# Kernel optimization log

Measured on AMD Instinct MI355X. Metric: run time of the kernel, lower is better.

Reference implementation:

```python
import jax, jax.numpy as jnp
import numpy as np

WEIGHT = 2.0  # penalty weight for |argmax - label| == 1 (original forward arg `weight`)
B, S, C = 64, 8192, 512


def setup_inputs() -> dict:
    key = jax.random.key(0)
    k1, k2 = jax.random.split(key)
    logits = jax.random.normal(k1, (B, S, C), dtype=jnp.float32)
    pre = jax.nn.log_softmax(logits, axis=-1)  # module expects log-softmax inputs
    y_true = jax.random.randint(k2, (B, S), 0, C)
    return {"pre": pre, "y_true": y_true}


def reference(pre, y_true):
    # gather log-prob of the true class: [B, S]
    gathered = jnp.take_along_axis(pre, y_true[..., None], axis=-1)[..., 0]
    # predicted class per position: [B, S]
    pred = jnp.argmax(pre, axis=-1)
    # penalize positions where prediction is off-by-one from the label
    mask = jnp.abs(pred - y_true) == 1
    total = jnp.sum(jnp.where(mask, WEIGHT * gathered, gathered))
    return total / pre.shape[0]
```

## Files before the change

kernel.cpp:

```cpp
#include <hip/hip_runtime.h>

#define NROWS (64 * 8192)
#define C 512
#define WEIGHT 2.0f
#define NBLOCKS 2048
#define BLOCK 256

__global__ __launch_bounds__(BLOCK) void nll_rows_kernel(
    const float* __restrict__ pre,
    const int* __restrict__ y_true,
    float* __restrict__ partial) {
    const int lane = threadIdx.x & 63;
    const int wave = threadIdx.x >> 6;
    const int gwave = blockIdx.x * 4 + wave;
    const int nwaves = gridDim.x * 4;

    float acc = 0.0f;

    for (int row = gwave; row < NROWS; row += nwaves) {
        const float4* rowp = reinterpret_cast<const float4*>(pre + (size_t)row * C);
        float4 a = rowp[lane];
        float4 b = rowp[64 + lane];

        int baseA = lane * 4;
        float mval = a.x; int midx = baseA;
        if (a.y > mval) { mval = a.y; midx = baseA + 1; }
        if (a.z > mval) { mval = a.z; midx = baseA + 2; }
        if (a.w > mval) { mval = a.w; midx = baseA + 3; }
        int baseB = 256 + lane * 4;
        if (b.x > mval) { mval = b.x; midx = baseB; }
        if (b.y > mval) { mval = b.y; midx = baseB + 1; }
        if (b.z > mval) { mval = b.z; midx = baseB + 2; }
        if (b.w > mval) { mval = b.w; midx = baseB + 3; }

        #pragma unroll
        for (int off = 1; off < 64; off <<= 1) {
            float oval = __shfl_xor(mval, off);
            int   oidx = __shfl_xor(midx, off);
            if (oval > mval || (oval == mval && oidx < midx)) {
                mval = oval; midx = oidx;
            }
        }

        int t = y_true[row];
        float g = pre[(size_t)row * C + t];
        int d = midx - t;
        float w = (d == 1 || d == -1) ? WEIGHT : 1.0f;
        if (lane == 0) acc += w * g;
    }

    __shared__ float ssum[4];
    if (lane == 0) ssum[wave] = acc;
    __syncthreads();
    if (threadIdx.x == 0) {
        partial[blockIdx.x] = ssum[0] + ssum[1] + ssum[2] + ssum[3];
    }
}

__global__ __launch_bounds__(256) void nll_reduce_kernel(
    const float* __restrict__ partial, float* __restrict__ out, int n) {
    __shared__ float s[256];
    float acc = 0.0f;
    for (int i = threadIdx.x; i < n; i += 256) acc += partial[i];
    s[threadIdx.x] = acc;
    __syncthreads();
    for (int w = 128; w > 0; w >>= 1) {
        if (threadIdx.x < w) s[threadIdx.x] += s[threadIdx.x + w];
        __syncthreads();
    }
    if (threadIdx.x == 0) out[0] = s[0] * (1.0f / 64.0f);
}

extern "C" void kernel_launch(void* const* d_in, const int* in_sizes, int n_in,
                              void* d_out, int out_size, void* d_ws, size_t ws_size,
                              hipStream_t stream) {
    const float* pre = (const float*)d_in[0];
    const int* y_true = (const int*)d_in[1];
    float* out = (float*)d_out;
    float* partial = (float*)d_ws;

    nll_rows_kernel<<<NBLOCKS, BLOCK, 0, stream>>>(pre, y_true, partial);
    nll_reduce_kernel<<<1, 256, 0, stream>>>(partial, out, NBLOCKS);
}
```

Baseline: 189.9 us.

## Process two rows per wave iteration with nontemporal loads and shuffle gather

Each wave now loads two rows per loop iteration using nontemporal vector loads, raising memory-level parallelism. The true-class log-prob is taken from registers via a wave shuffle instead of a separate global load. The loop trip count becomes a compile-time constant. This adds register pressure and assumes the row count divides evenly.

```diff
diff --git a/kernel.cpp b/kernel.cpp
--- a/kernel.cpp
+++ b/kernel.cpp
@@ -5,6 +5,48 @@
 #define WEIGHT 2.0f
 #define NBLOCKS 2048
 #define BLOCK 256
+#define NWAVES (NBLOCKS * 4)
+#define ITERS (NROWS / (2 * NWAVES))
+
+typedef float v4f __attribute__((ext_vector_type(4)));
+
+__device__ __forceinline__ void row_reduce(v4f a, v4f b, int lane, int t, float& acc) {
+    int baseA = lane * 4;
+    float mval = a.x; int midx = baseA;
+    if (a.y > mval) { mval = a.y; midx = baseA + 1; }
+    if (a.z > mval) { mval = a.z; midx = baseA + 2; }
+    if (a.w > mval) { mval = a.w; midx = baseA + 3; }
+    int baseB = 256 + lane * 4;
+    if (b.x > mval) { mval = b.x; midx = baseB; }
+    if (b.y > mval) { mval = b.y; midx = baseB + 1; }
+    if (b.z > mval) { mval = b.z; midx = baseB + 2; }
+    if (b.w > mval) { mval = b.w; midx = baseB + 3; }
+
+    #pragma unroll
+    for (int off = 1; off < 64; off <<= 1) {
+        float oval = __shfl_xor(mval, off);
+        int   oidx = __shfl_xor(midx, off);
+        if (oval > mval || (oval == mval && oidx < midx)) {
+            mval = oval; midx = oidx;
+        }
+    }
+
+    bool hi = t >= 256;
+    int  e = t & 3;
+    int  owner = (t & 255) >> 2;
+    float cx = hi ? b.x : a.x;
+    float cy = hi ? b.y : a.y;
+    float cz = hi ? b.z : a.z;
+    float cw = hi ? b.w : a.w;
+    float d0 = (e & 1) ? cy : cx;
+    float d1 = (e & 1) ? cw : cz;
+    float cand = (e & 2) ? d1 : d0;
+    float g = __shfl(cand, owner);
+
+    int d = midx - t;
+    float w = (d == 1 || d == -1) ? WEIGHT : 1.0f;
+    acc += w * g;
+}
 
 __global__ __launch_bounds__(BLOCK) void nll_rows_kernel(
     const float* __restrict__ pre,
@@ -13,40 +55,27 @@
     const int lane = threadIdx.x & 63;
     const int wave = threadIdx.x >> 6;
     const int gwave = blockIdx.x * 4 + wave;
-    const int nwaves = gridDim.x * 4;
+
+    const v4f* p = reinterpret_cast<const v4f*>(pre) + (size_t)gwave * (C / 4);
+    const size_t rstride = (size_t)NWAVES * (C / 4);
 
     float acc = 0.0f;
+    int row = gwave;
+    for (int it = 0; it < ITERS; ++it) {
+        const v4f* p0 = p;
+        const v4f* p1 = p + rstride;
+        v4f a0 = __builtin_nontemporal_load(p0 + lane);
+        v4f b0 = __builtin_nontemporal_load(p0 + 64 + lane);
+        v4f a1 = __builtin_nontemporal_load(p1 + lane);
+        v4f b1 = __builtin_nontemporal_load(p1 + 64 + lane);
+        int t0 = y_true[row];
+        int t1 = y_true[row + NWAVES];
 
-    for (int row = gwave; row < NROWS; row += nwaves) {
-        const float4* rowp = reinterpret_cast<const float4*>(pre + (size_t)row * C);
-        float4 a = rowp[lane];
-        float4 b = rowp[64 + lane];
+        row_reduce(a0, b0, lane, t0, acc);
+        row_reduce(a1, b1, lane, t1, acc);
 
-        int baseA = lane * 4;
-        float mval = a.x; int midx = baseA;
-        if (a.y > mval) { mval = a.y; midx = baseA + 1; }
-        if (a.z > mval) { mval = a.z; midx = baseA + 2; }
-        if (a.w > mval) { mval = a.w; midx = baseA + 3; }
-        int baseB = 256 + lane * 4;
-        if (b.x > mval) { mval = b.x; midx = baseB; }
-        if (b.y > mval) { mval = b.y; midx = baseB + 1; }
-        if (b.z > mval) { mval = b.z; midx = baseB + 2; }
-        if (b.w > mval) { mval = b.w; midx = baseB + 3; }
-
-        #pragma unroll
-        for (int off = 1; off < 64; off <<= 1) {
-            float oval = __shfl_xor(mval, off);
-            int   oidx = __shfl_xor(midx, off);
-            if (oval > mval || (oval == mval && oidx < midx)) {
-                mval = oval; midx = oidx;
-            }
-        }
-
-        int t = y_true[row];
-        float g = pre[(size_t)row * C + t];
-        int d = midx - t;
-        float w = (d == 1 || d == -1) ? WEIGHT : 1.0f;
-        if (lane == 0) acc += w * g;
+        p += 2 * rstride;
+        row += 2 * NWAVES;
     }
 
     __shared__ float ssum[4];
```

New measurement: 205.3 us. 8.1% more time.

## Replace shuffle argmax with DPP max, ballot first-index, and register gather

Applied to the files above, without the earlier changes.

The per-row argmax no longer carries (value, index) pairs through shuffle-xor rounds. It now takes a DPP wave max of values only, then finds the first matching index with ballot and ctz. The true-class log-prob is read from the row already held in registers via readlane, which removes the extra global gather load. The loop trip count is also fixed at compile time. This cuts cross-lane ALU and LDS-permute work in what is a memory-bound streaming kernel, and relies on the compare-equal tie-breaking matching the reference's first-index argmax.

```diff
diff --git a/kernel.cpp b/kernel.cpp
--- a/kernel.cpp
+++ b/kernel.cpp
@@ -5,6 +5,25 @@
 #define WEIGHT 2.0f
 #define NBLOCKS 2048
 #define BLOCK 256
+#define NWAVES (NBLOCKS * 4)
+#define ITERS (NROWS / NWAVES)
+
+typedef float v4f __attribute__((ext_vector_type(4)));
+
+__device__ __forceinline__ float dpp_wave_max(float v) {
+    const int NEGINF = 0xFF800000;
+#define DPP_STEP(ctrl)                                                        \
+    v = fmaxf(v, __int_as_float(__builtin_amdgcn_update_dpp(                  \
+                     NEGINF, __float_as_int(v), (ctrl), 0xf, 0xf, false)));
+    DPP_STEP(0x111)
+    DPP_STEP(0x112)
+    DPP_STEP(0x114)
+    DPP_STEP(0x118)
+    DPP_STEP(0x142)
+    DPP_STEP(0x143)
+#undef DPP_STEP
+    return v;
+}
 
 __global__ __launch_bounds__(BLOCK) void nll_rows_kernel(
     const float* __restrict__ pre,
@@ -13,40 +32,60 @@
     const int lane = threadIdx.x & 63;
     const int wave = threadIdx.x >> 6;
     const int gwave = blockIdx.x * 4 + wave;
-    const int nwaves = gridDim.x * 4;
 
     float acc = 0.0f;
 
-    for (int row = gwave; row < NROWS; row += nwaves) {
-        const float4* rowp = reinterpret_cast<const float4*>(pre + (size_t)row * C);
-        float4 a = rowp[lane];
-        float4 b = rowp[64 + lane];
+    int row = gwave;
+    for (int it = 0; it < ITERS; ++it, row += NWAVES) {
+        const v4f* rowp = reinterpret_cast<const v4f*>(pre + (size_t)row * C);
+        v4f a = rowp[lane];
+        v4f b = rowp[64 + lane];
+        int t = y_true[row];
 
-        int baseA = lane * 4;
-        float mval = a.x; int midx = baseA;
-        if (a.y > mval) { mval = a.y; midx = baseA + 1; }
-        if (a.z > mval) { mval = a.z; midx = baseA + 2; }
-        if (a.w > mval) { mval = a.w; midx = baseA + 3; }
-        int baseB = 256 + lane * 4;
-        if (b.x > mval) { mval = b.x; midx = baseB; }
-        if (b.y > mval) { mval = b.y; midx = baseB + 1; }
-        if (b.z > mval) { mval = b.z; midx = baseB + 2; }
-        if (b.w > mval) { mval = b.w; midx = baseB + 3; }
+        float m8 = fmaxf(fmaxf(fmaxf(a.x, a.y), fmaxf(a.z, a.w)),
+                         fmaxf(fmaxf(b.x, b.y), fmaxf(b.z, b.w)));
+        float vm = dpp_wave_max(m8);
+        float M = __int_as_float(__builtin_amdgcn_readlane(__float_as_int(vm), 63));
 
-        #pragma unroll
-        for (int off = 1; off < 64; off <<= 1) {
-            float oval = __shfl_xor(mval, off);
-            int   oidx = __shfl_xor(midx, off);
-            if (oval > mval || (oval == mval && oidx < midx)) {
-                mval = oval; midx = oidx;
-            }
+        int fA = 4;
+        if (a.w == M) fA = 3;
+        if (a.z == M) fA = 2;
+        if (a.y == M) fA = 1;
+        if (a.x == M) fA = 0;
+        int fB = 4;
+        if (b.w == M) fB = 3;
+        if (b.z == M) fB = 2;
+        if (b.y == M) fB = 1;
+        if (b.x == M) fB = 0;
+        unsigned long long mA = __ballot(fA < 4);
+        unsigned long long mB = __ballot(fB < 4);
+
+        int pred;
+        if (mA) {
+            int ol = __builtin_ctzll(mA);
+            pred = ol * 4 + __builtin_amdgcn_readlane(fA, ol);
+        } else {
+            int ol = __builtin_ctzll(mB);
+            pred = 256 + ol * 4 + __builtin_amdgcn_readlane(fB, ol);
         }
 
-        int t = y_true[row];
-        float g = pre[(size_t)row * C + t];
-        int d = midx - t;
+        int tu = __builtin_amdgcn_readfirstlane(t);
+        int e = tu & 3;
+        int owner = (tu & 255) >> 2;
+        bool hi = tu >= 256;
+        float cx = hi ? b.x : a.x;
+        float cy = hi ? b.y : a.y;
+        float cz = hi ? b.z : a.z;
+        float cw = hi ? b.w : a.w;
+        float d0 = (e & 1) ? cy : cx;
+        float d1 = (e & 1) ? cw : cz;
+        float cand = (e & 2) ? d1 : d0;
+        float g = __int_as_float(
+            __builtin_amdgcn_readlane(__float_as_int(cand), owner));
+
+        int d = pred - tu;
         float w = (d == 1 || d == -1) ? WEIGHT : 1.0f;
-        if (lane == 0) acc += w * g;
+        acc += w * g;
     }
 
     __shared__ float ssum[4];
```

Measured after the change: 197.5 us. 1.04x slower.
